# Optimization experiments

Measured on AMD Instinct MI355X. Metric: run time of the kernel, lower is better.

Reference implementation:

```python
import jax, jax.numpy as jnp
import numpy as np

N_HEADS = 16
HEAD_DIM = 64
D_MODEL = N_HEADS * HEAD_DIM  # 1024


def setup_inputs() -> dict:
    key = jax.random.key(0)
    ks = jax.random.split(key, 6)
    B, S, D = 2, 2048, D_MODEL
    s = 0.02
    return {
        "hidden_states": jax.random.normal(ks[0], (B, S, D), jnp.float32),
        "position_bias": jax.random.normal(ks[1], (1, N_HEADS, S, S), jnp.float32),
        "Wq": jax.random.normal(ks[2], (D, D), jnp.float32) * s,
        "Wk": jax.random.normal(ks[3], (D, D), jnp.float32) * s,
        "Wv": jax.random.normal(ks[4], (D, D), jnp.float32) * s,
        "Wo": jax.random.normal(ks[5], (D, D), jnp.float32) * s,
    }


def reference(hidden_states, position_bias, Wq, Wk, Wv, Wo):
    B, S, D = hidden_states.shape

    def split_heads(x):  # [B,S,D] -> [B,H,S,hd]
        return x.reshape(B, S, N_HEADS, HEAD_DIM).transpose(0, 2, 1, 3)

    q = split_heads(hidden_states @ Wq)
    k = split_heads(hidden_states @ Wk)
    v = split_heads(hidden_states @ Wv)

    # T5 attention: NO 1/sqrt(d) scaling; additive relative-position bias.
    scores = jnp.einsum("bhqd,bhkd->bhqk", q, k) + position_bias
    attn = jax.nn.softmax(scores.astype(jnp.float32), axis=-1).astype(scores.dtype)
    ctx = jnp.einsum("bhqk,bhkd->bhqd", attn, v)
    ctx = ctx.transpose(0, 2, 1, 3).reshape(B, S, D)
    return ctx @ Wo
```

## Files before the change

kernel.cpp:

```cpp
#include <hip/hip_runtime.h>
#include <hip/hip_bf16.h>
#include <stdint.h>

typedef __bf16 bf16_t;
typedef __bf16 bf16x4 __attribute__((ext_vector_type(4)));
typedef __bf16 bf16x8 __attribute__((ext_vector_type(8)));
typedef float  f32x4  __attribute__((ext_vector_type(4)));

#define S_LEN 2048
#define NH    16
#define HD    64
#define DM    1024
#define BATCH 2
#define M_TOT (BATCH * S_LEN)
#define SM_SHIFT 18.0f

__device__ __forceinline__ void gload16(const void* g, void* l) {
    __builtin_amdgcn_global_load_lds(
        (const __attribute__((address_space(1))) unsigned int*)g,
        (__attribute__((address_space(3))) unsigned int*)l, 16, 0, 0);
}

__global__ void convert_h(const float* __restrict__ X, bf16_t* __restrict__ Y, int n) {
    int i = (blockIdx.x * 256 + threadIdx.x) * 4;
    if (i >= n) return;
    float4 v = *(const float4*)(X + i);
    union { bf16_t h[4]; uint2 u; } pk;
    pk.h[0] = (bf16_t)v.x; pk.h[1] = (bf16_t)v.y;
    pk.h[2] = (bf16_t)v.z; pk.h[3] = (bf16_t)v.w;
    *(uint2*)(Y + i) = pk.u;
}

__global__ void convert_transpose_w4(const float* __restrict__ W0, const float* __restrict__ W1,
                                     const float* __restrict__ W2, const float* __restrict__ W3,
                                     bf16_t* __restrict__ D0, bf16_t* __restrict__ D3) {
    __shared__ float tile[32][33];
    const int z = blockIdx.z;
    const float* W = z == 0 ? W0 : z == 1 ? W1 : z == 2 ? W2 : W3;
    bf16_t* Wt = z < 3 ? D0 + (size_t)z * DM * DM : D3;
    const int tid = threadIdx.x;
    const int tx = tid & 31, ty = tid >> 5;
    const int bx = blockIdx.x * 32, by = blockIdx.y * 32;
#pragma unroll
    for (int it = 0; it < 4; ++it)
        tile[ty + it * 8][tx] = W[(size_t)(by + ty + it * 8) * DM + bx + tx];
    __syncthreads();
#pragma unroll
    for (int it = 0; it < 4; ++it)
        Wt[(size_t)(bx + ty + it * 8) * DM + by + tx] = (bf16_t)tile[tx][ty + it * 8];
}

template<int BN, int EPI>
__global__ __launch_bounds__(256)
void gemm_glds(const bf16_t* __restrict__ A, const bf16_t* __restrict__ Bt,
               float* __restrict__ Cf, bf16_t* __restrict__ Qb, bf16_t* __restrict__ Kb,
               bf16_t* __restrict__ Vtb, int M, int N, int K)
{
    constexpr int WN = BN / 2;
    constexpr int NJ = WN / 16;
    constexpr int RB = BN / 32;
    __shared__ bf16_t smem[16640];
    bf16_t* At  = smem;
    bf16_t* Bts = smem + 8192;

    const int tid  = threadIdx.x;
    const int lane = tid & 63;
    const int wave = tid >> 6;
    const int lc = lane & 15;
    const int l4 = lane >> 4;
    const int wr = wave >> 1, wc = wave & 1;
    const int m0 = blockIdx.y * 128;
    const int n0 = blockIdx.x * BN;
    const int srow = tid >> 3;
    const int scol = (tid & 7) * 8;

    f32x4 acc[4][NJ] = {};

    for (int k0 = 0; k0 < K; k0 += 64) {
        __syncthreads();
#pragma unroll
        for (int ro = 0; ro < 4; ++ro)
            gload16(A + (size_t)(m0 + ro * 32 + srow) * K + k0 + scol,
                    At + ro * 2048 + wave * 512);
#pragma unroll
        for (int ro = 0; ro < RB; ++ro)
            gload16(Bt + (size_t)(n0 + ro * 32 + srow) * K + k0 + scol,
                    Bts + ro * 2048 + wave * 512);
        __syncthreads();

        bf16x8 af[2][4], bfr[2][NJ];
#pragma unroll
        for (int kk = 0; kk < 2; ++kk) {
#pragma unroll
            for (int i = 0; i < 4; ++i)
                af[kk][i] = *(const bf16x8*)(At + (wr * 64 + i * 16 + lc) * 64 + kk * 32 + l4 * 8);
#pragma unroll
            for (int j = 0; j < NJ; ++j)
                bfr[kk][j] = *(const bf16x8*)(Bts + (wc * WN + j * 16 + lc) * 64 + kk * 32 + l4 * 8);
        }
#pragma unroll
        for (int kk = 0; kk < 2; ++kk)
#pragma unroll
            for (int i = 0; i < 4; ++i)
#pragma unroll
                for (int j = 0; j < NJ; ++j)
                    acc[i][j] = __builtin_amdgcn_mfma_f32_16x16x32_bf16(af[kk][i], bfr[kk][j], acc[i][j], 0, 0, 0);
    }

    if (EPI == 1) {
#pragma unroll
        for (int i = 0; i < 4; ++i)
#pragma unroll
            for (int j = 0; j < NJ; ++j)
#pragma unroll
                for (int r = 0; r < 4; ++r) {
                    int m = m0 + wr * 64 + i * 16 + l4 * 4 + r;
                    int n = n0 + wc * WN + j * 16 + lc;
                    Cf[(size_t)m * N + n] = acc[i][j][r];
                }
    } else {
        const int sel = n0 >> 10;
        if (sel < 2) {
            bf16_t* Dst = sel == 0 ? Qb : Kb;
#pragma unroll
            for (int i = 0; i < 4; ++i)
#pragma unroll
                for (int j = 0; j < NJ; ++j)
#pragma unroll
                    for (int r = 0; r < 4; ++r) {
                        int m = m0 + wr * 64 + i * 16 + l4 * 4 + r;
                        int n = (n0 & 1023) + wc * WN + j * 16 + lc;
                        int b = m >> 11, s = m & 2047, h = n >> 6, d = n & 63;
                        Dst[(((size_t)(b * NH + h)) * S_LEN + s) * HD + d] = (bf16_t)acc[i][j][r];
                    }
        } else {
            __syncthreads();
            bf16_t* Ct = smem;
#pragma unroll
            for (int i = 0; i < 4; ++i)
#pragma unroll
                for (int j = 0; j < NJ; ++j)
#pragma unroll
                    for (int r = 0; r < 4; ++r) {
                        int ml = wr * 64 + i * 16 + l4 * 4 + r;
                        int nl = wc * WN + j * 16 + lc;
                        Ct[nl * 130 + ml] = (bf16_t)acc[i][j][r];
                    }
            __syncthreads();
            const int rr = tid >> 1, c0 = (tid & 1) * 64;
            const int nn = (n0 - 2048) + rr;
            const int hh = nn >> 6, dd = nn & 63;
            const int bb = m0 >> 11, s0 = m0 & 2047;
            bf16_t* dst = Vtb + (((size_t)(bb * NH + hh)) * HD + dd) * S_LEN + s0 + c0;
            const bf16_t* srcr = Ct + rr * 130 + c0;
#pragma unroll
            for (int u = 0; u < 8; ++u)
                *(uint4*)(dst + u * 8) = *(const uint4*)(srcr + u * 8);
        }
    }
}

__global__ __launch_bounds__(512, 1)
void attn_kernel(const bf16_t* __restrict__ Q, const bf16_t* __restrict__ Kin,
                 const bf16_t* __restrict__ Vt, const float* __restrict__ bias,
                 bf16_t* __restrict__ Ctx)
{
    const int tid  = threadIdx.x;
    const int lane = tid & 63;
    const int wave = tid >> 6;
    const int b    = wave >> 2;
    const int ws   = wave & 3;
    const int lc = lane & 15;
    const int l4 = lane >> 4;

    const int f   = blockIdx.x;
    const int xcd = f & 7;
    const int kk_ = f >> 3;
    const int h   = xcd * 2 + (kk_ >> 4);
    const int qt  = kk_ & 15;
    const int qw  = qt * 128 + ws * 32;

    __shared__ bf16_t Kt[2][2][64 * 64];
    __shared__ bf16_t Vs[2][2][64 * 64];
    __shared__ float  Bs[2][128 * 64];

    const bf16_t* Qg = Q + (size_t)(b * NH + h) * S_LEN * HD;
    const bf16_t* Kg[2]; const bf16_t* Vg[2];
#pragma unroll
    for (int bb = 0; bb < 2; ++bb) {
        Kg[bb] = Kin + (size_t)(bb * NH + h) * S_LEN * HD;
        Vg[bb] = Vt  + (size_t)(bb * NH + h) * HD * S_LEN;
    }
    const float* Bg = bias + (size_t)h * S_LEN * S_LEN;

    bf16x8 qf[2][2];
#pragma unroll
    for (int i = 0; i < 2; ++i)
#pragma unroll
        for (int kk = 0; kk < 2; ++kk)
            qf[i][kk] = *(const bf16x8*)(Qg + (size_t)(qw + i * 16 + lc) * HD + kk * 32 + l4 * 8);

    f32x4 cacc[2][4] = {};
    float lsum[2] = {};

    const int r0   = lane >> 3;
    const int gsrc = (lane & 7) ^ r0;
    const int R    = wave * 8;

    auto stageKV = [&](int t, int pbuf) {
        const int kv0 = t * 64;
        gload16(Kg[0] + (size_t)(kv0 + R + r0) * HD + gsrc * 8, &Kt[0][pbuf][R * 64]);
        gload16(Kg[1] + (size_t)(kv0 + R + r0) * HD + gsrc * 8, &Kt[1][pbuf][R * 64]);
        gload16(Vg[0] + (size_t)(R + r0) * S_LEN + kv0 + gsrc * 8, &Vs[0][pbuf][R * 64]);
        gload16(Vg[1] + (size_t)(R + r0) * S_LEN + kv0 + gsrc * 8, &Vs[1][pbuf][R * 64]);
    };

    const int br4 = lane >> 4;
    const int bcg = lane & 15;
    auto stageB = [&](int t, int pbuf) {
        const int kv0 = t * 64;
#pragma unroll
        for (int c = 0; c < 4; ++c) {
            const int ql = wave * 16 + c * 4 + br4;
            const int sg = bcg ^ ((c & 1) * 4 + br4);
            gload16(Bg + (size_t)(qt * 128 + ql) * S_LEN + kv0 + sg * 4,
                    (char*)&Bs[pbuf][0] + (wave * 4 + c) * 1024);
        }
    };

    stageKV(0, 0);
    stageB(0, 0);
    __syncthreads();

    for (int t = 0; t < 32; ++t) {
        const int buf = t & 1;
        if (t < 31) {
            stageKV(t + 1, buf ^ 1);
            stageB(t + 1, buf ^ 1);
        }
        __builtin_amdgcn_sched_barrier(0);

        f32x4 saT[4][2] = {};
        __builtin_amdgcn_s_setprio(1);
#pragma unroll
        for (int kk = 0; kk < 2; ++kk) {
            bf16x8 kf[4];
#pragma unroll
            for (int j = 0; j < 4; ++j)
                kf[j] = *(const bf16x8*)(&Kt[b][buf][(j * 16 + lc) * 64 + (((kk * 4 + l4) ^ (lc & 7)) * 8)]);
#pragma unroll
            for (int j = 0; j < 4; ++j)
#pragma unroll
                for (int i = 0; i < 2; ++i)
                    saT[j][i] = __builtin_amdgcn_mfma_f32_16x16x32_bf16(kf[j], qf[i][kk], saT[j][i], 0, 0, 0);
        }
        __builtin_amdgcn_s_setprio(0);

        f32x4 bv[2][4];
        const float* Bbuf = &Bs[buf][0];
#pragma unroll
        for (int i = 0; i < 2; ++i)
#pragma unroll
            for (int j = 0; j < 4; ++j) {
                const int ql = ws * 32 + i * 16 + lc;
                bv[i][j] = *(const f32x4*)(Bbuf + ql * 64 + (((4 * j + l4) ^ (lc & 7)) * 4));
            }

        asm volatile("s_waitcnt lgkmcnt(0)" ::: "memory");
        __builtin_amdgcn_sched_barrier(0);
        __builtin_amdgcn_s_barrier();
        __builtin_amdgcn_sched_barrier(0);

        bf16_t* Pw = (bf16_t*)&Bs[buf][0] + ws * 4096 + b * 2048;

#pragma unroll
        for (int i = 0; i < 2; ++i) {
#pragma unroll
            for (int j = 0; j < 4; ++j) {
                f32x4 s = (saT[j][i] - SM_SHIFT) + bv[i][j];
                float p0 = __expf(s.x), p1 = __expf(s.y), p2 = __expf(s.z), p3 = __expf(s.w);
                lsum[i] += (p0 + p1) + (p2 + p3);
                bf16x4 pk = {(bf16_t)p0, (bf16_t)p1, (bf16_t)p2, (bf16_t)p3};
                *(bf16x4*)(Pw + (i * 16 + lc) * 64 + (((2 * j + (l4 >> 1)) ^ (lc & 7)) << 3) + 4 * (l4 & 1)) = pk;
            }
        }

        __builtin_amdgcn_s_setprio(1);
#pragma unroll
        for (int ks = 0; ks < 2; ++ks) {
            bf16x8 pf[2], vf[4];
#pragma unroll
            for (int i = 0; i < 2; ++i)
                pf[i] = *(const bf16x8*)(Pw + (i * 16 + lc) * 64 + (((4 * ks + l4) ^ (lc & 7)) << 3));
#pragma unroll
            for (int jd = 0; jd < 4; ++jd)
                vf[jd] = *(const bf16x8*)(&Vs[b][buf][(jd * 16 + lc) * 64 + (((ks * 4 + l4) ^ (lc & 7)) * 8)]);
#pragma unroll
            for (int i = 0; i < 2; ++i)
#pragma unroll
                for (int jd = 0; jd < 4; ++jd)
                    cacc[i][jd] = __builtin_amdgcn_mfma_f32_16x16x32_bf16(pf[i], vf[jd], cacc[i][jd], 0, 0, 0);
        }
        __builtin_amdgcn_s_setprio(0);

        __syncthreads();
    }

#pragma unroll
    for (int i = 0; i < 2; ++i) {
        lsum[i] += __shfl_xor(lsum[i], 16, 64);
        lsum[i] += __shfl_xor(lsum[i], 32, 64);
    }
    float rinv[2][4];
#pragma unroll
    for (int i = 0; i < 2; ++i)
#pragma unroll
        for (int r = 0; r < 4; ++r)
            rinv[i][r] = 1.0f / __shfl(lsum[i], l4 * 4 + r, 16);

    bf16_t* Co = Ctx + (size_t)b * S_LEN * DM + (size_t)h * HD;
#pragma unroll
    for (int i = 0; i < 2; ++i)
#pragma unroll
        for (int r = 0; r < 4; ++r) {
            int qrow = qw + i * 16 + l4 * 4 + r;
#pragma unroll
            for (int jd = 0; jd < 4; ++jd)
                Co[(size_t)qrow * DM + jd * 16 + lc] = (bf16_t)(cacc[i][jd][r] * rinv[i][r]);
        }
}

extern "C" void kernel_launch(void* const* d_in, const int* in_sizes, int n_in,
                              void* d_out, int out_size, void* d_ws, size_t ws_size,
                              hipStream_t stream)
{
    (void)in_sizes; (void)n_in; (void)out_size; (void)ws_size;
    const float* hs   = (const float*)d_in[0];
    const float* bias = (const float*)d_in[1];
    const float* Wq   = (const float*)d_in[2];
    const float* Wk   = (const float*)d_in[3];
    const float* Wv   = (const float*)d_in[4];
    const float* Wo   = (const float*)d_in[5];
    float* out = (float*)d_out;

    char* ws = (char*)d_ws;
    bf16_t* Hbf   = (bf16_t*)(ws);
    bf16_t* Wqkvt = (bf16_t*)(ws + ( 8u << 20));
    bf16_t* Wot   = (bf16_t*)(ws + (14u << 20));
    bf16_t* Qb    = (bf16_t*)(ws + (16u << 20));
    bf16_t* Kb    = (bf16_t*)(ws + (24u << 20));
    bf16_t* Vtb   = (bf16_t*)(ws + (32u << 20));
    bf16_t* Ctx   = (bf16_t*)(ws + (40u << 20));

    convert_h<<<4096, 256, 0, stream>>>(hs, Hbf, M_TOT * DM);
    dim3 tg(32, 32, 4);
    convert_transpose_w4<<<tg, 256, 0, stream>>>(Wq, Wk, Wv, Wo, Wqkvt, Wot);

    dim3 gq(3 * DM / 128, M_TOT / 128);
    gemm_glds<128, 0><<<gq, 256, 0, stream>>>(Hbf, Wqkvt, nullptr, Qb, Kb, Vtb,
                                              M_TOT, 3 * DM, DM);

    attn_kernel<<<256, 512, 0, stream>>>(Qb, Kb, Vtb, bias, Ctx);

    dim3 go(DM / 64, M_TOT / 128);
    gemm_glds<64, 1><<<go, 256, 0, stream>>>(Ctx, Wot, out, nullptr, nullptr, nullptr,
                                             M_TOT, DM, DM);
}
```

Before: 189.6 us.

## Keep softmax probabilities in registers and use one barrier per KV tile

The exponentiated scores are packed to bf16 in registers with v_cvt_pk_bf16_f32 and fed directly as the A operand of the PV MFMA. This removes the round trip that wrote P to LDS and read it back. V fragments are now read as two 4-element halves so their k-ordering matches the register layout of P. The two barriers per iteration are merged into one at the top of the loop, which waits on vmcnt and lgkmcnt before prefetching the next tile. The risks are more VGPR pressure and possible stalls from the full vmcnt wait.

```diff
diff --git a/kernel.cpp b/kernel.cpp
--- a/kernel.cpp
+++ b/kernel.cpp
@@ -230,31 +230,19 @@
 
     stageKV(0, 0);
     stageB(0, 0);
-    __syncthreads();
 
     for (int t = 0; t < 32; ++t) {
         const int buf = t & 1;
+        __builtin_amdgcn_sched_barrier(0);
+        asm volatile("s_waitcnt lgkmcnt(0)" ::: "memory");
+        asm volatile("s_waitcnt vmcnt(0)" ::: "memory");
+        __builtin_amdgcn_s_barrier();
+        __builtin_amdgcn_sched_barrier(0);
         if (t < 31) {
             stageKV(t + 1, buf ^ 1);
             stageB(t + 1, buf ^ 1);
         }
         __builtin_amdgcn_sched_barrier(0);
-
-        f32x4 saT[4][2] = {};
-        __builtin_amdgcn_s_setprio(1);
-#pragma unroll
-        for (int kk = 0; kk < 2; ++kk) {
-            bf16x8 kf[4];
-#pragma unroll
-            for (int j = 0; j < 4; ++j)
-                kf[j] = *(const bf16x8*)(&Kt[b][buf][(j * 16 + lc) * 64 + (((kk * 4 + l4) ^ (lc & 7)) * 8)]);
-#pragma unroll
-            for (int j = 0; j < 4; ++j)
-#pragma unroll
-                for (int i = 0; i < 2; ++i)
-                    saT[j][i] = __builtin_amdgcn_mfma_f32_16x16x32_bf16(kf[j], qf[i][kk], saT[j][i], 0, 0, 0);
-        }
-        __builtin_amdgcn_s_setprio(0);
 
         f32x4 bv[2][4];
         const float* Bbuf = &Bs[buf][0];
@@ -266,44 +254,57 @@
                 bv[i][j] = *(const f32x4*)(Bbuf + ql * 64 + (((4 * j + l4) ^ (lc & 7)) * 4));
             }
 
-        asm volatile("s_waitcnt lgkmcnt(0)" ::: "memory");
-        __builtin_amdgcn_sched_barrier(0);
-        __builtin_amdgcn_s_barrier();
-        __builtin_amdgcn_sched_barrier(0);
-
-        bf16_t* Pw = (bf16_t*)&Bs[buf][0] + ws * 4096 + b * 2048;
-
+        f32x4 saT[4][2] = {};
+        __builtin_amdgcn_s_setprio(1);
+#pragma unroll
+        for (int kk = 0; kk < 2; ++kk) {
+            bf16x8 kf[4];
+#pragma unroll
+            for (int j = 0; j < 4; ++j)
+                kf[j] = *(const bf16x8*)(&Kt[b][buf][(j * 16 + lc) * 64 + (((kk * 4 + l4) ^ (lc & 7)) * 8)]);
+#pragma unroll
+            for (int j = 0; j < 4; ++j)
+#pragma unroll
+                for (int i = 0; i < 2; ++i)
+                    saT[j][i] = __builtin_amdgcn_mfma_f32_16x16x32_bf16(kf[j], qf[i][kk], saT[j][i], 0, 0, 0);
+        }
+        __builtin_amdgcn_s_setprio(0);
+
+        union { uint32_t d[4]; bf16x8 v; } pa[2][2];
 #pragma unroll
         for (int i = 0; i < 2; ++i) {
+            f32x4 pe[4];
 #pragma unroll
             for (int j = 0; j < 4; ++j) {
                 f32x4 s = (saT[j][i] - SM_SHIFT) + bv[i][j];
-                float p0 = __expf(s.x), p1 = __expf(s.y), p2 = __expf(s.z), p3 = __expf(s.w);
-                lsum[i] += (p0 + p1) + (p2 + p3);
-                bf16x4 pk = {(bf16_t)p0, (bf16_t)p1, (bf16_t)p2, (bf16_t)p3};
-                *(bf16x4*)(Pw + (i * 16 + lc) * 64 + (((2 * j + (l4 >> 1)) ^ (lc & 7)) << 3) + 4 * (l4 & 1)) = pk;
+                pe[j].x = __expf(s.x); pe[j].y = __expf(s.y);
+                pe[j].z = __expf(s.z); pe[j].w = __expf(s.w);
+                lsum[i] += (pe[j].x + pe[j].y) + (pe[j].z + pe[j].w);
             }
+#pragma unroll
+            for (int ks = 0; ks < 2; ++ks) {
+                asm("v_cvt_pk_bf16_f32 %0, %1, %2" : "=v"(pa[i][ks].d[0]) : "v"(pe[2*ks].x),   "v"(pe[2*ks].y));
+                asm("v_cvt_pk_bf16_f32 %0, %1, %2" : "=v"(pa[i][ks].d[1]) : "v"(pe[2*ks].z),   "v"(pe[2*ks].w));
+                asm("v_cvt_pk_bf16_f32 %0, %1, %2" : "=v"(pa[i][ks].d[2]) : "v"(pe[2*ks+1].x), "v"(pe[2*ks+1].y));
+                asm("v_cvt_pk_bf16_f32 %0, %1, %2" : "=v"(pa[i][ks].d[3]) : "v"(pe[2*ks+1].z), "v"(pe[2*ks+1].w));
+            }
         }
 
         __builtin_amdgcn_s_setprio(1);
 #pragma unroll
         for (int ks = 0; ks < 2; ++ks) {
-            bf16x8 pf[2], vf[4];
-#pragma unroll
-            for (int i = 0; i < 2; ++i)
-                pf[i] = *(const bf16x8*)(Pw + (i * 16 + lc) * 64 + (((4 * ks + l4) ^ (lc & 7)) << 3));
-#pragma unroll
-            for (int jd = 0; jd < 4; ++jd)
-                vf[jd] = *(const bf16x8*)(&Vs[b][buf][(jd * 16 + lc) * 64 + (((ks * 4 + l4) ^ (lc & 7)) * 8)]);
-#pragma unroll
-            for (int i = 0; i < 2; ++i)
-#pragma unroll
-                for (int jd = 0; jd < 4; ++jd)
-                    cacc[i][jd] = __builtin_amdgcn_mfma_f32_16x16x32_bf16(pf[i], vf[jd], cacc[i][jd], 0, 0, 0);
+#pragma unroll
+            for (int jd = 0; jd < 4; ++jd) {
+                union { bf16x4 h[2]; bf16x8 v; } vv;
+                const int row = jd * 16 + lc;
+                vv.h[0] = *(const bf16x4*)(&Vs[b][buf][row * 64 + (((4 * ks +     (l4 >> 1)) ^ (lc & 7)) * 8) + 4 * (l4 & 1)]);
+                vv.h[1] = *(const bf16x4*)(&Vs[b][buf][row * 64 + (((4 * ks + 2 + (l4 >> 1)) ^ (lc & 7)) * 8) + 4 * (l4 & 1)]);
+#pragma unroll
+                for (int i = 0; i < 2; ++i)
+                    cacc[i][jd] = __builtin_amdgcn_mfma_f32_16x16x32_bf16(pa[i][ks].v, vv.v, cacc[i][jd], 0, 0, 0);
+            }
         }
         __builtin_amdgcn_s_setprio(0);
-
-        __syncthreads();
     }
 
 #pragma unroll
```

New measurement: 182.0 us. 1.04x faster.
